# Kernel tuning notes

Measured on AMD Instinct MI355X. Metric: run time of the kernel, lower is better.

The kernel has to match this reference:

```python
import jax, jax.numpy as jnp
import numpy as np

N = 50000   # nodes
E = 600000  # edges / hyperedge incidences
D = 128     # node_in_dim
H = 128     # hidden_dim
TAU = 0.5
ALPHA = 0.5
LAM = 0.5

_PARAM_SHAPES = [('Wq0', (1, H)), ('bq0', (H,)), ('W0', (D, H)), ('b0', (H,)),
                 ('Whq0', (1, H)), ('bhq0', (H,)), ('Wh0', (D, H)), ('bh0', (H,)),
                 ('Wf0', (H, H)), ('bf0', (H,)), ('Wfh0', (H, H)), ('bfh0', (H,)),
                 ('aq0', (H,)), ('a0', (H,)), ('ahq0', (H,)), ('ah0', (H,)),
                 ('aq_', (H,)), ('a_', (H,)), ('ahq_', (H,)), ('ah_', (H,)),
                 ('Wlq', (1, H)), ('blq', (H,)), ('Wlf', (D, H)), ('blf', (H,)),
                 ('Wm1', (H, H)), ('bm1', (H,)), ('Wm2', (H, H)), ('bm2', (H,))]


def setup_inputs() -> dict:
    key = jax.random.key(0)
    ks = jax.random.split(key, 8 + len(_PARAM_SHAPES))
    inp = {}
    inp['feats'] = jax.random.normal(ks[0], (N, D), dtype=jnp.float32)
    inp['edge_index'] = jax.random.randint(ks[1], (2, E), 0, N).astype(jnp.int32)
    inp['edge_index_aug'] = jax.random.randint(ks[2], (2, E), 0, N).astype(jnp.int32)
    inp['pos'] = jax.random.randint(ks[3], (100,), 1, N).astype(jnp.int32)
    inp['q'] = 0
    for i, (nm, sh) in enumerate(_PARAM_SHAPES):
        inp[nm] = jax.random.normal(ks[4 + i], sh, dtype=jnp.float32) * 0.05
    return inp


def _forward(feats, Wq0, bq0, W0, b0, Whq0, bhq0, Wh0, bh0, Wf0, bf0, Wfh0, bfh0,
             aq0, a0, ahq0, ah0, aq_, a_, ahq_, ah_, Wlq, blq, Wlf, blf,
             Wm1, bm1, Wm2, bm2, edge_index, edge_index_aug, q, pos):
    # ---- GCNConv (PyG default: add self-loops + symmetric normalization) ----
    sl = jnp.arange(N, dtype=edge_index.dtype)
    src = jnp.concatenate([edge_index[0], sl])
    dst = jnp.concatenate([edge_index[1], sl])
    deg = jax.ops.segment_sum(jnp.ones(src.shape[0], jnp.float32), dst, num_segments=N)
    dinv = jax.lax.rsqrt(deg)  # deg >= 1 thanks to self-loops
    enorm = dinv[src] * dinv[dst]

    def gcn(x, W, b):
        xw = x @ W
        return jax.ops.segment_sum(xw[src] * enorm[:, None], dst, num_segments=N) + b

    # ---- HypergraphConv (PyG, no attention): X' = D^-1 H B^-1 H^T X W ----
    node = edge_index_aug[0]
    he = edge_index_aug[1]
    Be = jax.ops.segment_sum(jnp.ones((E,), jnp.float32), he, num_segments=N)
    Dn = jax.ops.segment_sum(jnp.ones((E,), jnp.float32), node, num_segments=N)
    Binv = jnp.where(Be > 0, 1.0 / Be, 0.0)
    Dninv = jnp.where(Dn > 0, 1.0 / Dn, 0.0)

    def hg(x, W, b):
        xw = x @ W
        me = jax.ops.segment_sum(xw[node], he, num_segments=N) * Binv[:, None]
        return jax.ops.segment_sum(me[he], node, num_segments=N) * Dninv[:, None] + b

    # ---- attention-weighted fusion of two views (softmax over 2 logits) ----
    def fuse(a, b, wa, wb):
        att = jax.nn.softmax(jnp.stack([a @ wa, b @ wb], axis=1), axis=1)  # [N,2]
        return att[:, 0:1] * a + att[:, 1:2] * b

    querys = jnp.zeros((N, 1), jnp.float32).at[q].set(1.0)
    hq = jax.nn.relu(gcn(querys, Wq0, bq0))
    h = jax.nn.relu(gcn(feats, W0, b0))
    hf = fuse(hq, h, aq0, a0)
    h_augq = jax.nn.relu(hg(querys, Whq0, bhq0))
    h_aug = jax.nn.relu(hg(feats, Wh0, bh0))
    h_augf = fuse(h_augq, h_aug, ahq0, ah0)
    querys2 = querys @ Wlq + blq
    feats2 = feats @ Wlf + blf
    hf_ = fuse(querys2, feats2, aq_, a_)
    hf = jax.nn.relu(hf + gcn(hf_, Wf0, bf0))
    hfh_ = fuse(querys2, feats2, ahq_, ah_)
    h_augf = jax.nn.relu(h_augf + hg(hfh_, Wfh0, bfh0))

    def mlp(x):
        return jax.nn.relu(x @ Wm1 + bm1) @ Wm2 + bm2

    z = mlp(hf)
    z_aug = mlp(h_augf)

    # ---- Contra loss ----
    def expcos(v, M):
        num = M @ v
        den = jnp.maximum(jnp.linalg.norm(M, axis=1) * jnp.linalg.norm(v), 1e-8)
        return jnp.exp(num / den / TAU)

    sim1 = expcos(z[q], z)
    sim_aug1 = expcos(z_aug[q], z_aug)
    sim2 = expcos(z[q], z_aug)
    sim_aug2 = expcos(z_aug[q], z)
    mask = jnp.zeros((N,), bool).at[pos].set(True).at[q].set(False)
    nmask = jnp.sum(mask).astype(jnp.float32)

    def nlm(s):  # mean over positives of -log(s_i / sum(s))
        r = jnp.log(jnp.sum(s)) - jnp.log(s)
        return jnp.sum(jnp.where(mask, r, 0.0)) / nmask

    loss_intra = 0.5 * (nlm(sim1) + nlm(sim_aug1))
    loss_inter = 0.5 * (nlm(sim2) + nlm(sim_aug2))
    z_unsup = jnp.log(jnp.sum(sim2)) - jnp.log(sim2[q])
    z_aug_unsup = jnp.log(jnp.sum(sim_aug2)) - jnp.log(sim_aug2[q])
    loss_unsup = 0.5 * z_unsup + 0.5 * z_aug_unsup
    return loss_intra + ALPHA * loss_inter + LAM * loss_unsup


def reference(feats, Wq0, bq0, W0, b0, Whq0, bhq0, Wh0, bh0, Wf0, bf0, Wfh0, bfh0,
              aq0, a0, ahq0, ah0, aq_, a_, ahq_, ah_, Wlq, blq, Wlf, blf,
              Wm1, bm1, Wm2, bm2, edge_index, edge_index_aug, q, pos):
    return _forward(feats, Wq0, bq0, W0, b0, Whq0, bhq0, Wh0, bh0, Wf0, bf0, Wfh0, bfh0,
                    aq0, a0, ahq0, ah0, aq_, a_, ahq_, ah_, Wlq, blq, Wlf, blf,
                    Wm1, bm1, Wm2, bm2, edge_index, edge_index_aug, q, pos)
```

## Files before the change

### kernel.cpp

```cpp
#include <hip/hip_runtime.h>

#define NN 50000
#define EE 600000
#define HH 128
#define TAU_INV 2.0f
#define PSZ 6250
#define CAP 48

typedef __attribute__((ext_vector_type(8))) short short8;
typedef __attribute__((ext_vector_type(4))) float f32x4;
typedef __attribute__((ext_vector_type(2))) float floatx2;

__device__ __forceinline__ float wsum64(float v) {
#pragma unroll
  for (int m = 32; m >= 1; m >>= 1) v += __shfl_xor(v, m, 64);
  return v;
}
__device__ __forceinline__ unsigned short f2bf(float f) {
  unsigned u = __builtin_bit_cast(unsigned, f);
  u = u + 0x7FFFu + ((u >> 16) & 1u);
  return (unsigned short)(u >> 16);
}
__device__ __forceinline__ float bf2f(unsigned short h) {
  unsigned u = ((unsigned)h) << 16;
  return __builtin_bit_cast(float, u);
}
__device__ __forceinline__ unsigned char fp8_enc1(float v) {
  int p = __builtin_amdgcn_cvt_pk_fp8_f32(v, v, 0, false);
  return (unsigned char)(p & 0xFF);
}
__device__ __forceinline__ void fp8x8_dec(uint2 v, float* f) {
  floatx2 a = __builtin_amdgcn_cvt_pk_f32_fp8(v.x, false);
  floatx2 b = __builtin_amdgcn_cvt_pk_f32_fp8(v.x, true);
  floatx2 c = __builtin_amdgcn_cvt_pk_f32_fp8(v.y, false);
  floatx2 d = __builtin_amdgcn_cvt_pk_f32_fp8(v.y, true);
  f[0] = a.x; f[1] = a.y; f[2] = b.x; f[3] = b.y;
  f[4] = c.x; f[5] = c.y; f[6] = d.x; f[7] = d.y;
}
__device__ __forceinline__ uint2 fp8x8_enc(const float* f) {
  int w0 = __builtin_amdgcn_cvt_pk_fp8_f32(f[0], f[1], 0, false);
  w0 = __builtin_amdgcn_cvt_pk_fp8_f32(f[2], f[3], w0, true);
  int w1 = __builtin_amdgcn_cvt_pk_fp8_f32(f[4], f[5], 0, false);
  w1 = __builtin_amdgcn_cvt_pk_fp8_f32(f[6], f[7], w1, true);
  return make_uint2((unsigned)w0, (unsigned)w1);
}

__global__ void fill_k(const int* __restrict__ ei, const int* __restrict__ ea,
                       const int* __restrict__ qp, int* __restrict__ cursor,
                       unsigned short* __restrict__ slotsA, unsigned short* __restrict__ slotsB,
                       unsigned short* __restrict__ slotsC, float* __restrict__ cntq) {
  const int p = blockIdx.x & 7;
  const int lo = p * PSZ, hi = lo + PSZ;
  const int q = *qp;
  const int stride = (gridDim.x >> 3) * 256;
  for (int e = (blockIdx.x >> 3) * 256 + threadIdx.x; e < EE; e += stride) {
    int src = ei[e], dst = ei[EE + e];
    if (dst >= lo && dst < hi) {
      int idx = atomicAdd(&cursor[dst], 1);
      if (idx < CAP) slotsA[dst * CAP + idx] = (unsigned short)src;
    }
    int node = ea[e], he = ea[EE + e];
    if (he >= lo && he < hi) {
      int idx = atomicAdd(&cursor[NN + he], 1);
      if (idx < CAP) slotsB[he * CAP + idx] = (unsigned short)node;
      if (node == q) atomicAdd(&cntq[he], 1.0f);
    }
    if (node >= lo && node < hi) {
      int idx = atomicAdd(&cursor[2 * NN + node], 1);
      if (idx < CAP) slotsC[node * CAP + idx] = (unsigned short)he;
    }
  }
}

__global__ void derive_k(const int* __restrict__ cursor, float* __restrict__ dinv,
                         float* __restrict__ Binv, float* __restrict__ Dninv,
                         const int* __restrict__ pos, const int* __restrict__ qp,
                         int* __restrict__ maskI) {
  int i = blockIdx.x * 256 + threadIdx.x;
  if (i < NN) {
    dinv[i] = rsqrtf((float)(cursor[i] + 1));
    int b = cursor[NN + i];
    Binv[i] = (b > 0) ? 1.0f / (float)b : 0.0f;
    int d = cursor[2 * NN + i];
    Dninv[i] = (d > 0) ? 1.0f / (float)d : 0.0f;
  }
  if (blockIdx.x == 0) {
    int t = threadIdx.x;
    if (t < 100) maskI[pos[t]] = 1;
    __syncthreads();
    if (t == 0) maskI[*qp] = 0;
  }
}

__global__ void shq_k(const int* __restrict__ ei, const int* __restrict__ ea,
                      const int* __restrict__ qp, const float* __restrict__ dinv,
                      const float* __restrict__ Binv, const float* __restrict__ cntq,
                      float* __restrict__ s_hq, float* __restrict__ s_hgq) {
  int e = blockIdx.x * 256 + threadIdx.x;
  if (e >= EE) return;
  int q = *qp;
  int src = ei[e];
  if (src == q) {
    int dst = ei[EE + e];
    atomicAdd(&s_hq[dst], dinv[q] * dinv[dst]);
  }
  int he = ea[EE + e];
  float cq = cntq[he];
  if (cq != 0.0f) {
    int node = ea[e];
    atomicAdd(&s_hgq[node], Binv[he] * cq);
  }
  if (e == 0) atomicAdd(&s_hq[q], dinv[q] * dinv[q]);
}

__global__ void pack_k(const float* __restrict__ W0, const float* __restrict__ Wh0,
                       const float* __restrict__ Wlf, const float* __restrict__ Wf0,
                       const float* __restrict__ Wfh0, const float* __restrict__ Wm1,
                       const float* __restrict__ Wm2, unsigned short* __restrict__ out) {
  int tid = blockIdx.x * 256 + threadIdx.x;
  if (tid >= 7 * 2048) return;
  int mat = tid >> 11, r = tid & 2047;
  int s = r >> 9, c = (r >> 6) & 7, lane = r & 63;
  const float* W = (mat == 0) ? W0 : (mat == 1) ? Wh0 : (mat == 2) ? Wlf
                 : (mat == 3) ? Wf0 : (mat == 4) ? Wfh0 : (mat == 5) ? Wm1 : Wm2;
  int k0 = 32 * s + (lane >> 4) * 8;
  int n = 16 * c + (lane & 15);
  unsigned short* o = out + (size_t)tid * 8;
#pragma unroll
  for (int j = 0; j < 8; ++j) o[j] = f2bf(W[(k0 + j) * 128 + n]);
}

#define LDSW 136

template <bool BIAS, bool RELU, int OM>
__device__ __forceinline__ void gemm_core(const unsigned short* As, const short8* Wp,
                                          const float* bias, void* outv, int r0, int nrows,
                                          int tid) {
  const int wave = tid >> 6, lane = tid & 63;
  const int quad = lane >> 4, l15 = lane & 15;
  const int rw = r0 + wave * 16;
  f32x4 acc[8];
#pragma unroll
  for (int c = 0; c < 8; ++c) acc[c] = (f32x4){0.f, 0.f, 0.f, 0.f};
#pragma unroll
  for (int s = 0; s < 4; ++s) {
    short8 a = *(const short8*)&As[(wave * 16 + l15) * LDSW + s * 32 + quad * 8];
#pragma unroll
    for (int c = 0; c < 8; ++c) {
      short8 b = Wp[(s * 8 + c) * 64 + lane];
      acc[c] = __builtin_amdgcn_mfma_f32_16x16x32_bf16(a, b, acc[c], 0, 0, 0);
    }
  }
#pragma unroll
  for (int c = 0; c < 8; ++c) {
    int col = c * 16 + l15;
    float bv = BIAS ? bias[col] : 0.f;
#pragma unroll
    for (int r = 0; r < 4; ++r) {
      int grow = rw + quad * 4 + r;
      if (grow < nrows) {
        float v = acc[c][r] + bv;
        if (RELU) v = fmaxf(v, 0.f);
        if (OM == 2)
          ((unsigned char*)outv)[(size_t)grow * 256 + col] = fp8_enc1(v);
        else if (OM == 1)
          ((unsigned short*)outv)[(size_t)grow * 128 + col] = f2bf(v);
        else
          ((float*)outv)[(size_t)grow * 128 + col] = v;
      }
    }
  }
}

__device__ __forceinline__ void stage_bf16(const unsigned short* A, unsigned short* As,
                                           int r0, int nrows, int tid) {
#pragma unroll
  for (int t = 0; t < 4; ++t) {
    int v = t * 256 + tid;
    int row = v >> 4, cc = v & 15;
    int gr = r0 + row;
    uint4 val = make_uint4(0, 0, 0, 0);
    if (gr < nrows) val = ((const uint4*)A)[(size_t)gr * 16 + cc];
    *(uint4*)&As[row * LDSW + cc * 8] = val;
  }
}

template <bool BIAS, bool RELU, int OM>
__global__ __launch_bounds__(256) void gemm2_mfma(const unsigned short* __restrict__ A0,
                                                  const unsigned short* __restrict__ A1,
                                                  const short8* __restrict__ Wp0,
                                                  const short8* __restrict__ Wp1,
                                                  const float* __restrict__ b0,
                                                  const float* __restrict__ b1,
                                                  void* __restrict__ o0, void* __restrict__ o1,
                                                  int nrows, int nblk) {
  __shared__ unsigned short As[64 * LDSW];
  int b = blockIdx.x;
  const unsigned short* A = A0;
  const short8* Wp = Wp0;
  const float* bias = b0;
  void* o = o0;
  if (b >= nblk) {
    b -= nblk; A = A1; Wp = Wp1; bias = b1; o = o1;
  }
  const int r0 = b * 64;
  stage_bf16(A, As, r0, nrows, threadIdx.x);
  __syncthreads();
  gemm_core<BIAS, RELU, OM>(As, Wp, bias, o, r0, nrows, threadIdx.x);
}

__global__ __launch_bounds__(256) void gemm3_mfma(const float* __restrict__ A,
                                                  const short8* __restrict__ Wp,
                                                  const float* __restrict__ bias2,
                                                  unsigned char* __restrict__ p1,
                                                  unsigned char* __restrict__ p2,
                                                  unsigned short* __restrict__ out2,
                                                  int nrows) {
  __shared__ unsigned short As[64 * LDSW];
  const int tid = threadIdx.x;
  const int r0 = blockIdx.x * 64;
#pragma unroll
  for (int t = 0; t < 8; ++t) {
    int v = t * 256 + tid;
    int row = v >> 5, c4 = v & 31;
    int gr = r0 + row;
    float4 val = make_float4(0.f, 0.f, 0.f, 0.f);
    if (gr < nrows) val = ((const float4*)A)[(size_t)gr * 32 + c4];
    ushort4 o;
    o.x = f2bf(val.x); o.y = f2bf(val.y); o.z = f2bf(val.z); o.w = f2bf(val.w);
    *(ushort4*)&As[row * LDSW + c4 * 4] = o;
  }
  __syncthreads();
  const int wave = tid >> 6, lane = tid & 63;
  const int quad = lane >> 4, l15 = lane & 15;
  const int rw = r0 + wave * 16;
  f32x4 acc[3][8];
#pragma unroll
  for (int m = 0; m < 3; ++m)
#pragma unroll
    for (int c = 0; c < 8; ++c) acc[m][c] = (f32x4){0.f, 0.f, 0.f, 0.f};
#pragma unroll
  for (int s = 0; s < 4; ++s) {
    short8 a = *(const short8*)&As[(wave * 16 + l15) * LDSW + s * 32 + quad * 8];
#pragma unroll
    for (int m = 0; m < 3; ++m)
#pragma unroll
      for (int c = 0; c < 8; ++c) {
        short8 b = Wp[(size_t)m * 2048 + (s * 8 + c) * 64 + lane];
        acc[m][c] = __builtin_amdgcn_mfma_f32_16x16x32_bf16(a, b, acc[m][c], 0, 0, 0);
      }
  }
#pragma unroll
  for (int c = 0; c < 8; ++c) {
    int col = c * 16 + l15;
    float bv = bias2[col];
#pragma unroll
    for (int r = 0; r < 4; ++r) {
      int grow = rw + quad * 4 + r;
      if (grow < nrows) {
        p1[(size_t)grow * 256 + col] = fp8_enc1(acc[0][c][r]);
        p2[(size_t)grow * 256 + col] = fp8_enc1(acc[1][c][r]);
        out2[(size_t)grow * 128 + col] = f2bf(acc[2][c][r] + bv);
      }
    }
  }
}

template <int MODE, bool OUTFP8>
__device__ __forceinline__ void gpair_body(const uint2* __restrict__ xp,
                                           unsigned short* __restrict__ y1,
                                           unsigned short* __restrict__ y2,
                                           uint2* __restrict__ yp,
                                           const int* __restrict__ cnt,
                                           const unsigned short* __restrict__ slots,
                                           const float* __restrict__ wv, int blk) {
  int node = blk * 8 + (threadIdx.x >> 5);
  if (node >= NN) return;
  int l = threadIdx.x & 31;
  int st = node * CAP;
  int n = min(cnt[node], CAP);
  float acc[8];
#pragma unroll
  for (int i = 0; i < 8; ++i) acc[i] = 0.f;
  int p = 0;
  for (; p + 4 <= n; p += 4) {
    ushort4 s4 = *(const ushort4*)&slots[st + p];
    uint2 v0 = xp[(size_t)s4.x * 32 + l];
    uint2 v1 = xp[(size_t)s4.y * 32 + l];
    uint2 v2 = xp[(size_t)s4.z * 32 + l];
    uint2 v3 = xp[(size_t)s4.w * 32 + l];
    float f[8];
    if (MODE == 0) {
      float w0 = wv[s4.x], w1 = wv[s4.y], w2 = wv[s4.z], w3 = wv[s4.w];
      fp8x8_dec(v0, f);
#pragma unroll
      for (int i = 0; i < 8; ++i) acc[i] = fmaf(w0, f[i], acc[i]);
      fp8x8_dec(v1, f);
#pragma unroll
      for (int i = 0; i < 8; ++i) acc[i] = fmaf(w1, f[i], acc[i]);
      fp8x8_dec(v2, f);
#pragma unroll
      for (int i = 0; i < 8; ++i) acc[i] = fmaf(w2, f[i], acc[i]);
      fp8x8_dec(v3, f);
#pragma unroll
      for (int i = 0; i < 8; ++i) acc[i] = fmaf(w3, f[i], acc[i]);
    } else {
      fp8x8_dec(v0, f);
#pragma unroll
      for (int i = 0; i < 8; ++i) acc[i] += f[i];
      fp8x8_dec(v1, f);
#pragma unroll
      for (int i = 0; i < 8; ++i) acc[i] += f[i];
      fp8x8_dec(v2, f);
#pragma unroll
      for (int i = 0; i < 8; ++i) acc[i] += f[i];
      fp8x8_dec(v3, f);
#pragma unroll
      for (int i = 0; i < 8; ++i) acc[i] += f[i];
    }
  }
  for (; p < n; ++p) {
    int s = slots[st + p];
    uint2 v = xp[(size_t)s * 32 + l];
    float f[8];
    fp8x8_dec(v, f);
    if (MODE == 0) {
      float w = wv[s];
#pragma unroll
      for (int i = 0; i < 8; ++i) acc[i] = fmaf(w, f[i], acc[i]);
    } else {
#pragma unroll
      for (int i = 0; i < 8; ++i) acc[i] += f[i];
    }
  }
  float sc = wv[node];
  if (MODE == 0) {
    uint2 v = xp[(size_t)node * 32 + l];
    float f[8];
    fp8x8_dec(v, f);
#pragma unroll
    for (int i = 0; i < 8; ++i) acc[i] = sc * fmaf(sc, f[i], acc[i]);
  } else {
#pragma unroll
    for (int i = 0; i < 8; ++i) acc[i] *= sc;
  }
  if (OUTFP8) {
    yp[(size_t)node * 32 + l] = fp8x8_enc(acc);
  } else {
    unsigned short* y = (l < 16) ? y1 : y2;
    int cg = l & 15;
    uint4 o;
    o.x = ((unsigned)f2bf(acc[1]) << 16) | f2bf(acc[0]);
    o.y = ((unsigned)f2bf(acc[3]) << 16) | f2bf(acc[2]);
    o.z = ((unsigned)f2bf(acc[5]) << 16) | f2bf(acc[4]);
    o.w = ((unsigned)f2bf(acc[7]) << 16) | f2bf(acc[6]);
    *(uint4*)&y[(size_t)node * 128 + cg * 8] = o;
  }
}

__global__ void dgather12_k(const uint2* __restrict__ xp1, unsigned short* __restrict__ y1a,
                            unsigned short* __restrict__ y1b, const uint2* __restrict__ xp2,
                            uint2* __restrict__ yp3, const int* __restrict__ cursor,
                            const unsigned short* __restrict__ slotsA,
                            const unsigned short* __restrict__ slotsB,
                            const float* __restrict__ dinv, const float* __restrict__ Binv,
                            int nblk) {
  int b = blockIdx.x;
  if (b < nblk)
    gpair_body<0, false>(xp1, y1a, y1b, nullptr, cursor, slotsA, dinv, b);
  else
    gpair_body<1, true>(xp2, nullptr, nullptr, yp3, cursor + NN, slotsB, Binv, b - nblk);
}

__global__ void dgather3_k(const uint2* __restrict__ xp, unsigned short* __restrict__ y1,
                           unsigned short* __restrict__ y2, const int* __restrict__ cursor,
                           const unsigned short* __restrict__ slotsC,
                           const float* __restrict__ wv) {
  gpair_body<1, false>(xp, y1, y2, nullptr, cursor + 2 * NN, slotsC, wv, blockIdx.x);
}

__device__ __forceinline__ void fuse_add_body(const unsigned short* __restrict__ g,
                                              const unsigned short* __restrict__ gr,
                                              const float* __restrict__ svec,
                                              const float* __restrict__ dscale,
                                              const float* __restrict__ Wq,
                                              const float* __restrict__ bq,
                                              const float* __restrict__ bm,
                                              const float* __restrict__ aq,
                                              const float* __restrict__ am,
                                              const float* __restrict__ bres,
                                              unsigned short* __restrict__ out, int blk) {
  int row = blk * 4 + (threadIdx.x >> 6);
  if (row >= NN) return;
  int lane = threadIdx.x & 63;
  int c0 = lane, c1 = lane + 64;
  float s = svec[row];
  if (dscale) s *= dscale[row];
  float hq0 = fmaxf(fmaf(s, Wq[c0], bq[c0]), 0.f);
  float hq1 = fmaxf(fmaf(s, Wq[c1], bq[c1]), 0.f);
  float h0 = fmaxf(bf2f(g[(size_t)row * 128 + c0]) + bm[c0], 0.f);
  float h1 = fmaxf(bf2f(g[(size_t)row * 128 + c1]) + bm[c1], 0.f);
  float dq = wsum64(hq0 * aq[c0] + hq1 * aq[c1]);
  float dm = wsum64(h0 * am[c0] + h1 * am[c1]);
  float mx = fmaxf(dq, dm);
  float e0 = expf(dq - mx), e1 = expf(dm - mx);
  float w0 = e0 / (e0 + e1), w1 = 1.f - w0;
  float r0 = fmaxf(w0 * hq0 + w1 * h0 + bf2f(gr[(size_t)row * 128 + c0]) + bres[c0], 0.f);
  float r1 = fmaxf(w0 * hq1 + w1 * h1 + bf2f(gr[(size_t)row * 128 + c1]) + bres[c1], 0.f);
  out[(size_t)row * 128 + c0] = f2bf(r0);
  out[(size_t)row * 128 + c1] = f2bf(r1);
}

__global__ void fuse_add2_k(const unsigned short* gA, const unsigned short* grA,
                            const float* svA, const float* dsA, const float* WqA,
                            const float* bqA, const float* bmA, const float* aqA,
                            const float* amA, const float* brA, unsigned short* outA,
                            const unsigned short* gB, const unsigned short* grB,
                            const float* svB, const float* dsB, const float* WqB,
                            const float* bqB, const float* bmB, const float* aqB,
                            const float* amB, const float* brB, unsigned short* outB,
                            int nblk) {
  int b = blockIdx.x;
  if (b < nblk)
    fuse_add_body(gA, grA, svA, dsA, WqA, bqA, bmA, aqA, amA, brA, outA, b);
  else
    fuse_add_body(gB, grB, svB, dsB, WqB, bqB, bmB, aqB, amB, brB, outB, b - nblk);
}

__global__ void fuse2_k(const unsigned short* __restrict__ f2, const int* __restrict__ qp,
                        const float* __restrict__ Wlq, const float* __restrict__ blq,
                        const float* __restrict__ aq1, const float* __restrict__ a1,
                        const float* __restrict__ aq2, const float* __restrict__ a2,
                        unsigned short* __restrict__ out1, unsigned short* __restrict__ out2) {
  int row = blockIdx.x * 4 + (threadIdx.x >> 6);
  if (row >= NN) return;
  int lane = threadIdx.x & 63;
  int c0 = lane, c1 = lane + 64;
  int q = *qp;
  float q20 = blq[c0] + ((row == q) ? Wlq[c0] : 0.f);
  float q21 = blq[c1] + ((row == q) ? Wlq[c1] : 0.f);
  float f0 = bf2f(f2[(size_t)row * 128 + c0]);
  float f1 = bf2f(f2[(size_t)row * 128 + c1]);
  float dq1 = wsum64(q20 * aq1[c0] + q21 * aq1[c1]);
  float df1 = wsum64(f0 * a1[c0] + f1 * a1[c1]);
  float dq2 = wsum64(q20 * aq2[c0] + q21 * aq2[c1]);
  float df2 = wsum64(f0 * a2[c0] + f1 * a2[c1]);
  {
    float mx = fmaxf(dq1, df1);
    float e0 = expf(dq1 - mx), e1 = expf(df1 - mx);
    float w0 = e0 / (e0 + e1), w1 = 1.f - w0;
    out1[(size_t)row * 128 + c0] = f2bf(w0 * q20 + w1 * f0);
    out1[(size_t)row * 128 + c1] = f2bf(w0 * q21 + w1 * f1);
  }
  {
    float mx = fmaxf(dq2, df2);
    float e0 = expf(dq2 - mx), e1 = expf(df2 - mx);
    float w0 = e0 / (e0 + e1), w1 = 1.f - w0;
    out2[(size_t)row * 128 + c0] = f2bf(w0 * q20 + w1 * f0);
    out2[(size_t)row * 128 + c1] = f2bf(w0 * q21 + w1 * f1);
  }
}

__global__ void sim_k(const unsigned short* __restrict__ z,
                      const unsigned short* __restrict__ za, const int* __restrict__ qp,
                      float4* __restrict__ simbuf, float* __restrict__ scal_out) {
  int row = blockIdx.x * 4 + (threadIdx.x >> 6);
  if (row >= NN) return;
  int lane = threadIdx.x & 63;
  int c0 = lane, c1 = lane + 64;
  int q = *qp;
  float zi0 = bf2f(z[(size_t)row * 128 + c0]), zi1 = bf2f(z[(size_t)row * 128 + c1]);
  float zai0 = bf2f(za[(size_t)row * 128 + c0]), zai1 = bf2f(za[(size_t)row * 128 + c1]);
  float zq0 = bf2f(z[(size_t)q * 128 + c0]), zq1 = bf2f(z[(size_t)q * 128 + c1]);
  float zaq0 = bf2f(za[(size_t)q * 128 + c0]), zaq1 = bf2f(za[(size_t)q * 128 + c1]);
  float nzi = wsum64(zi0 * zi0 + zi1 * zi1);
  float nzai = wsum64(zai0 * zai0 + zai1 * zai1);
  float nzq = wsum64(zq0 * zq0 + zq1 * zq1);
  float nzaq = wsum64(zaq0 * zaq0 + zaq1 * zaq1);
  float d1 = wsum64(zi0 * zq0 + zi1 * zq1);
  float d2 = wsum64(zai0 * zaq0 + zai1 * zaq1);
  float d3 = wsum64(zai0 * zq0 + zai1 * zq1);
  float d4 = wsum64(zi0 * zaq0 + zi1 * zaq1);
  if (lane == 0) {
    float ni = sqrtf(nzi), nai = sqrtf(nzai);
    float nq = sqrtf(nzq), naq = sqrtf(nzaq);
    float c1_ = d1 / fmaxf(ni * nq, 1e-8f) * TAU_INV;
    float ca1 = d2 / fmaxf(nai * naq, 1e-8f) * TAU_INV;
    float c2_ = d3 / fmaxf(nai * nq, 1e-8f) * TAU_INV;
    float ca2 = d4 / fmaxf(ni * naq, 1e-8f) * TAU_INV;
    simbuf[row] = make_float4(c1_, ca1, c2_, ca2);
    if (row == q) {
      scal_out[9] = c2_;
      scal_out[10] = ca2;
    }
  }
}

__global__ __launch_bounds__(256) void reduce_sim_k(const float4* __restrict__ simbuf,
                                                    const int* __restrict__ maskI,
                                                    float* __restrict__ scal) {
  float acc[9];
#pragma unroll
  for (int i = 0; i < 9; ++i) acc[i] = 0.f;
  for (int row = blockIdx.x * 256 + threadIdx.x; row < NN; row += gridDim.x * 256) {
    float4 v = simbuf[row];
    acc[0] += expf(v.x);
    acc[1] += expf(v.y);
    acc[2] += expf(v.z);
    acc[3] += expf(v.w);
    if (maskI[row]) {
      acc[4] += v.x; acc[5] += v.y; acc[6] += v.z; acc[7] += v.w;
      acc[8] += 1.0f;
    }
  }
  __shared__ float s[9][4];
  int lane = threadIdx.x & 63, wv = threadIdx.x >> 6;
#pragma unroll
  for (int i = 0; i < 9; ++i) {
    float r = wsum64(acc[i]);
    if (lane == 0) s[i][wv] = r;
  }
  __syncthreads();
  if (threadIdx.x < 9) {
    float r = s[threadIdx.x][0] + s[threadIdx.x][1] + s[threadIdx.x][2] + s[threadIdx.x][3];
    atomicAdd(&scal[threadIdx.x], r);
  }
}

__global__ void final_k(const float* __restrict__ scal, float* __restrict__ out) {
  if (threadIdx.x != 0 || blockIdx.x != 0) return;
  float S1 = scal[0], Sa1 = scal[1], S2 = scal[2], Sa2 = scal[3];
  float L1 = scal[4], La1 = scal[5], L2 = scal[6], La2 = scal[7];
  float NM = scal[8], Q2 = scal[9], Qa2 = scal[10];
  float intra = 0.5f * ((logf(S1) - L1 / NM) + (logf(Sa1) - La1 / NM));
  float inter = 0.5f * ((logf(S2) - L2 / NM) + (logf(Sa2) - La2 / NM));
  float unsup = 0.5f * (logf(S2) - Q2) + 0.5f * (logf(Sa2) - Qa2);
  out[0] = intra + 0.5f * inter + 0.5f * unsup;
}

extern "C" void kernel_launch(void* const* d_in, const int* in_sizes, int n_in,
                              void* d_out, int out_size, void* d_ws, size_t ws_size,
                              hipStream_t stream) {
  const float* feats = (const float*)d_in[0];
  const int* ei = (const int*)d_in[1];
  const int* ea = (const int*)d_in[2];
  const int* pos = (const int*)d_in[3];
  const int* qp = (const int*)d_in[4];
  const float* Wq0 = (const float*)d_in[5];
  const float* bq0 = (const float*)d_in[6];
  const float* W0 = (const float*)d_in[7];
  const float* b0 = (const float*)d_in[8];
  const float* Whq0 = (const float*)d_in[9];
  const float* bhq0 = (const float*)d_in[10];
  const float* Wh0 = (const float*)d_in[11];
  const float* bh0 = (const float*)d_in[12];
  const float* Wf0 = (const float*)d_in[13];
  const float* bf0 = (const float*)d_in[14];
  const float* Wfh0 = (const float*)d_in[15];
  const float* bfh0 = (const float*)d_in[16];
  const float* aq0 = (const float*)d_in[17];
  const float* a0 = (const float*)d_in[18];
  const float* ahq0 = (const float*)d_in[19];
  const float* ah0 = (const float*)d_in[20];
  const float* aq_ = (const float*)d_in[21];
  const float* a_ = (const float*)d_in[22];
  const float* ahq_ = (const float*)d_in[23];
  const float* ah_ = (const float*)d_in[24];
  const float* Wlq = (const float*)d_in[25];
  const float* blq = (const float*)d_in[26];
  const float* Wlf = (const float*)d_in[27];
  const float* blf = (const float*)d_in[28];
  const float* Wm1 = (const float*)d_in[29];
  const float* bm1 = (const float*)d_in[30];
  const float* Wm2 = (const float*)d_in[31];
  const float* bm2 = (const float*)d_in[32];

  char* ws = (char*)d_ws;
  size_t off = 0;
  auto take = [&](size_t bytes) -> void* {
    void* p = ws + off;
    off = (off + bytes + 255) & ~(size_t)255;
    return p;
  };
  int* cursor3 = (int*)take(3 * NN * 4);
  int* maskI = (int*)take(NN * 4);
  float* s_hq = (float*)take(NN * 4);
  float* cntq = (float*)take(NN * 4);
  float* s_hgq = (float*)take(NN * 4);
  float* scal = (float*)take(64 * 4);
  size_t zero_end = off;
  unsigned short* slotsA = (unsigned short*)take((size_t)NN * CAP * 2);
  unsigned short* slotsB = (unsigned short*)take((size_t)NN * CAP * 2);
  unsigned short* slotsC = (unsigned short*)take((size_t)NN * CAP * 2);
  float* dinv = (float*)take(NN * 4);
  float* Binv = (float*)take(NN * 4);
  float* Dninv = (float*)take(NN * 4);
  float4* simbuf = (float4*)take((size_t)NN * 16);
  unsigned short* Wpack = (unsigned short*)take((size_t)7 * 16384 * 2);
  const size_t BFSZ = (size_t)NN * HH * 2;
  unsigned short* B0 = (unsigned short*)take(BFSZ);
  unsigned short* B1 = (unsigned short*)take(BFSZ);
  unsigned short* B2 = (unsigned short*)take(BFSZ);
  unsigned short* B3 = (unsigned short*)take(BFSZ);
  unsigned short* B4 = (unsigned short*)take(BFSZ);
  unsigned short* B5 = (unsigned short*)take(BFSZ);
  unsigned short* B6 = (unsigned short*)take(BFSZ);
  unsigned char* P1 = (unsigned char*)take((size_t)NN * 256);
  unsigned char* P2 = (unsigned char*)take((size_t)NN * 256);
  unsigned char* P3 = (unsigned char*)take((size_t)NN * 256);

  const int NB = (NN + 255) / 256;
  const int EB = (EE + 255) / 256;
  const int GMB = (NN + 63) / 64;
  const int GTB = (NN + 7) / 8;
  const int RB = (NN + 3) / 4;
  const short8* Wp = (const short8*)Wpack;

  hipMemsetAsync(d_ws, 0, zero_end, stream);
  fill_k<<<4096, 256, 0, stream>>>(ei, ea, qp, cursor3, slotsA, slotsB, slotsC, cntq);
  derive_k<<<NB, 256, 0, stream>>>(cursor3, dinv, Binv, Dninv, pos, qp, maskI);
  shq_k<<<EB, 256, 0, stream>>>(ei, ea, qp, dinv, Binv, cntq, s_hq, s_hgq);

  pack_k<<<(7 * 2048 + 255) / 256, 256, 0, stream>>>(W0, Wh0, Wlf, Wf0, Wfh0, Wm1, Wm2,
                                                     Wpack);
  gemm3_mfma<<<GMB, 256, 0, stream>>>(feats, Wp, blf, P1, P2, B6, NN);
  fuse2_k<<<RB, 256, 0, stream>>>(B6, qp, Wlq, blq, aq_, a_, ahq_, ah_, B3, B4);
  gemm2_mfma<false, false, 2><<<2 * GMB, 256, 0, stream>>>(
      B3, B4, Wp + (size_t)3 * 2048, Wp + (size_t)4 * 2048, nullptr, nullptr, P1 + 128,
      P2 + 128, NN, GMB);
  dgather12_k<<<2 * GTB, 256, 0, stream>>>((const uint2*)P1, B0, B1, (const uint2*)P2,
                                           (uint2*)P3, cursor3, slotsA, slotsB, dinv, Binv,
                                           GTB);
  dgather3_k<<<GTB, 256, 0, stream>>>((const uint2*)P3, B2, B5, cursor3, slotsC, Dninv);
  fuse_add2_k<<<2 * RB, 256, 0, stream>>>(
      B0, B1, s_hq, nullptr, Wq0, bq0, b0, aq0, a0, bf0, B3,
      B2, B5, s_hgq, Dninv, Whq0, bhq0, bh0, ahq0, ah0, bfh0, B4, RB);
  gemm2_mfma<true, true, 1><<<2 * GMB, 256, 0, stream>>>(
      B3, B4, Wp + (size_t)5 * 2048, Wp + (size_t)5 * 2048, bm1, bm1, B0, B1, NN, GMB);
  gemm2_mfma<true, false, 1><<<2 * GMB, 256, 0, stream>>>(
      B0, B1, Wp + (size_t)6 * 2048, Wp + (size_t)6 * 2048, bm2, bm2, B2, B5, NN, GMB);
  sim_k<<<RB, 256, 0, stream>>>(B2, B5, qp, simbuf, scal);
  reduce_sim_k<<<64, 256, 0, stream>>>(simbuf, maskI, scal);
  final_k<<<1, 64, 0, stream>>>(scal, (float*)d_out);
}
```

Baseline: 477.1 us.

## Merge independent stages into shared launches and pad slot stride to 64

Independent stages now share launches so they overlap on the device: weight packing with edge-slot filling, the feature GEMM with degree derivation and the query-score pass, the third gather with the first fuse-add, and the second fuse-add with the first MLP GEMM. The query-score pass now derives its normalization from the cursor counts directly, so it no longer has to wait for a separate derive kernel. The MLP GEMMs are rescheduled into a staggered pipeline, and the RELU flag becomes a runtime argument. The per-node slot stride is padded from 48 to 64 entries for aligned gather rows. The aim is to cut launch count and idle tails; the cost is more branching inside kernels, heterogeneous blocks sharing a grid, and a larger slot buffer.

Result: no change. 477.2 us (+0.0%).

```diff
diff --git a/kernel.cpp b/kernel.cpp
--- a/kernel.cpp
+++ b/kernel.cpp
@@ -6,6 +6,7 @@
 #define TAU_INV 2.0f
 #define PSZ 6250
 #define CAP 48
+#define SSTR 64
 
 typedef __attribute__((ext_vector_type(8))) short short8;
 typedef __attribute__((ext_vector_type(4))) float f32x4;
@@ -45,79 +46,48 @@
   return make_uint2((unsigned)w0, (unsigned)w1);
 }
 
-__global__ void fill_k(const int* __restrict__ ei, const int* __restrict__ ea,
-                       const int* __restrict__ qp, int* __restrict__ cursor,
-                       unsigned short* __restrict__ slotsA, unsigned short* __restrict__ slotsB,
-                       unsigned short* __restrict__ slotsC, float* __restrict__ cntq) {
-  const int p = blockIdx.x & 7;
+#define LDSW 136
+
+
+__device__ __forceinline__ void fill_body(const int* __restrict__ ei,
+                                          const int* __restrict__ ea,
+                                          const int* __restrict__ qp, int* __restrict__ cursor,
+                                          unsigned short* __restrict__ slotsA,
+                                          unsigned short* __restrict__ slotsB,
+                                          unsigned short* __restrict__ slotsC,
+                                          float* __restrict__ cntq, int blk, int nblk) {
+  const int p = blk & 7;
   const int lo = p * PSZ, hi = lo + PSZ;
   const int q = *qp;
-  const int stride = (gridDim.x >> 3) * 256;
-  for (int e = (blockIdx.x >> 3) * 256 + threadIdx.x; e < EE; e += stride) {
+  const int stride = (nblk >> 3) * 256;
+  for (int e = (blk >> 3) * 256 + threadIdx.x; e < EE; e += stride) {
     int src = ei[e], dst = ei[EE + e];
     if (dst >= lo && dst < hi) {
       int idx = atomicAdd(&cursor[dst], 1);
-      if (idx < CAP) slotsA[dst * CAP + idx] = (unsigned short)src;
+      if (idx < CAP) slotsA[dst * SSTR + idx] = (unsigned short)src;
     }
     int node = ea[e], he = ea[EE + e];
     if (he >= lo && he < hi) {
       int idx = atomicAdd(&cursor[NN + he], 1);
-      if (idx < CAP) slotsB[he * CAP + idx] = (unsigned short)node;
+      if (idx < CAP) slotsB[he * SSTR + idx] = (unsigned short)node;
       if (node == q) atomicAdd(&cntq[he], 1.0f);
     }
     if (node >= lo && node < hi) {
       int idx = atomicAdd(&cursor[2 * NN + node], 1);
-      if (idx < CAP) slotsC[node * CAP + idx] = (unsigned short)he;
-    }
-  }
-}
-
-__global__ void derive_k(const int* __restrict__ cursor, float* __restrict__ dinv,
-                         float* __restrict__ Binv, float* __restrict__ Dninv,
-                         const int* __restrict__ pos, const int* __restrict__ qp,
-                         int* __restrict__ maskI) {
-  int i = blockIdx.x * 256 + threadIdx.x;
-  if (i < NN) {
-    dinv[i] = rsqrtf((float)(cursor[i] + 1));
-    int b = cursor[NN + i];
-    Binv[i] = (b > 0) ? 1.0f / (float)b : 0.0f;
-    int d = cursor[2 * NN + i];
-    Dninv[i] = (d > 0) ? 1.0f / (float)d : 0.0f;
-  }
-  if (blockIdx.x == 0) {
-    int t = threadIdx.x;
-    if (t < 100) maskI[pos[t]] = 1;
-    __syncthreads();
-    if (t == 0) maskI[*qp] = 0;
-  }
-}
-
-__global__ void shq_k(const int* __restrict__ ei, const int* __restrict__ ea,
-                      const int* __restrict__ qp, const float* __restrict__ dinv,
-                      const float* __restrict__ Binv, const float* __restrict__ cntq,
-                      float* __restrict__ s_hq, float* __restrict__ s_hgq) {
-  int e = blockIdx.x * 256 + threadIdx.x;
-  if (e >= EE) return;
-  int q = *qp;
-  int src = ei[e];
-  if (src == q) {
-    int dst = ei[EE + e];
-    atomicAdd(&s_hq[dst], dinv[q] * dinv[dst]);
-  }
-  int he = ea[EE + e];
-  float cq = cntq[he];
-  if (cq != 0.0f) {
-    int node = ea[e];
-    atomicAdd(&s_hgq[node], Binv[he] * cq);
-  }
-  if (e == 0) atomicAdd(&s_hq[q], dinv[q] * dinv[q]);
-}
-
-__global__ void pack_k(const float* __restrict__ W0, const float* __restrict__ Wh0,
-                       const float* __restrict__ Wlf, const float* __restrict__ Wf0,
-                       const float* __restrict__ Wfh0, const float* __restrict__ Wm1,
-                       const float* __restrict__ Wm2, unsigned short* __restrict__ out) {
-  int tid = blockIdx.x * 256 + threadIdx.x;
+      if (idx < CAP) slotsC[node * SSTR + idx] = (unsigned short)he;
+    }
+  }
+}
+
+__device__ __forceinline__ void pack_body(const float* __restrict__ W0,
+                                          const float* __restrict__ Wh0,
+                                          const float* __restrict__ Wlf,
+                                          const float* __restrict__ Wf0,
+                                          const float* __restrict__ Wfh0,
+                                          const float* __restrict__ Wm1,
+                                          const float* __restrict__ Wm2,
+                                          unsigned short* __restrict__ out, int blk) {
+  int tid = blk * 256 + threadIdx.x;
   if (tid >= 7 * 2048) return;
   int mat = tid >> 11, r = tid & 2047;
   int s = r >> 9, c = (r >> 6) & 7, lane = r & 63;
@@ -130,12 +100,56 @@
   for (int j = 0; j < 8; ++j) o[j] = f2bf(W[(k0 + j) * 128 + n]);
 }
 
-#define LDSW 136
-
-template <bool BIAS, bool RELU, int OM>
-__device__ __forceinline__ void gemm_core(const unsigned short* As, const short8* Wp,
-                                          const float* bias, void* outv, int r0, int nrows,
-                                          int tid) {
+__device__ __forceinline__ void derive_body(const int* __restrict__ cursor,
+                                            float* __restrict__ dinv, float* __restrict__ Binv,
+                                            float* __restrict__ Dninv,
+                                            const int* __restrict__ pos,
+                                            const int* __restrict__ qp,
+                                            int* __restrict__ maskI, int blk) {
+  int i = blk * 256 + threadIdx.x;
+  if (i < NN) {
+    dinv[i] = rsqrtf((float)(cursor[i] + 1));
+    int b = cursor[NN + i];
+    Binv[i] = (b > 0) ? 1.0f / (float)b : 0.0f;
+    int d = cursor[2 * NN + i];
+    Dninv[i] = (d > 0) ? 1.0f / (float)d : 0.0f;
+  }
+  if (blk == 0) {
+    int t = threadIdx.x;
+    if (t < 100) maskI[pos[t]] = 1;
+    __syncthreads();
+    if (t == 0) maskI[*qp] = 0;
+  }
+}
+
+__device__ __forceinline__ void shq_body(const int* __restrict__ ei, const int* __restrict__ ea,
+                                         const int* __restrict__ qp,
+                                         const int* __restrict__ cursor,
+                                         const float* __restrict__ cntq,
+                                         float* __restrict__ s_hq, float* __restrict__ s_hgq,
+                                         int blk) {
+  int e = blk * 256 + threadIdx.x;
+  if (e >= EE) return;
+  int q = *qp;
+  int src = ei[e];
+  if (src == q) {
+    int dst = ei[EE + e];
+    float dq = rsqrtf((float)(cursor[q] + 1));
+    atomicAdd(&s_hq[dst], dq * rsqrtf((float)(cursor[dst] + 1)));
+  }
+  int he = ea[EE + e];
+  float cq = cntq[he];
+  if (cq != 0.0f) {
+    int node = ea[e];
+    atomicAdd(&s_hgq[node], cq / (float)cursor[NN + he]);
+  }
+  if (e == 0) atomicAdd(&s_hq[q], 1.0f / (float)(cursor[q] + 1));
+}
+
+template <bool BIAS, int OM>
+__device__ __forceinline__ void gemm_core_rt(const unsigned short* As, const short8* Wp,
+                                             const float* bias, void* outv, int r0, int nrows,
+                                             int tid, int relu) {
   const int wave = tid >> 6, lane = tid & 63;
   const int quad = lane >> 4, l15 = lane & 15;
   const int rw = r0 + wave * 16;
@@ -160,13 +174,11 @@
       int grow = rw + quad * 4 + r;
       if (grow < nrows) {
         float v = acc[c][r] + bv;
-        if (RELU) v = fmaxf(v, 0.f);
+        if (relu) v = fmaxf(v, 0.f);
         if (OM == 2)
           ((unsigned char*)outv)[(size_t)grow * 256 + col] = fp8_enc1(v);
-        else if (OM == 1)
+        else
           ((unsigned short*)outv)[(size_t)grow * 128 + col] = f2bf(v);
-        else
-          ((float*)outv)[(size_t)grow * 128 + col] = v;
       }
     }
   }
@@ -185,40 +197,15 @@
   }
 }
 
-template <bool BIAS, bool RELU, int OM>
-__global__ __launch_bounds__(256) void gemm2_mfma(const unsigned short* __restrict__ A0,
-                                                  const unsigned short* __restrict__ A1,
-                                                  const short8* __restrict__ Wp0,
-                                                  const short8* __restrict__ Wp1,
-                                                  const float* __restrict__ b0,
-                                                  const float* __restrict__ b1,
-                                                  void* __restrict__ o0, void* __restrict__ o1,
-                                                  int nrows, int nblk) {
-  __shared__ unsigned short As[64 * LDSW];
-  int b = blockIdx.x;
-  const unsigned short* A = A0;
-  const short8* Wp = Wp0;
-  const float* bias = b0;
-  void* o = o0;
-  if (b >= nblk) {
-    b -= nblk; A = A1; Wp = Wp1; bias = b1; o = o1;
-  }
-  const int r0 = b * 64;
-  stage_bf16(A, As, r0, nrows, threadIdx.x);
-  __syncthreads();
-  gemm_core<BIAS, RELU, OM>(As, Wp, bias, o, r0, nrows, threadIdx.x);
-}
-
-__global__ __launch_bounds__(256) void gemm3_mfma(const float* __restrict__ A,
-                                                  const short8* __restrict__ Wp,
-                                                  const float* __restrict__ bias2,
-                                                  unsigned char* __restrict__ p1,
-                                                  unsigned char* __restrict__ p2,
-                                                  unsigned short* __restrict__ out2,
-                                                  int nrows) {
-  __shared__ unsigned short As[64 * LDSW];
+__device__ __forceinline__ void gemm3_body(unsigned short* As, const float* __restrict__ A,
+                                           const short8* __restrict__ Wp,
+                                           const float* __restrict__ bias2,
+                                           unsigned char* __restrict__ p1,
+                                           unsigned char* __restrict__ p2,
+                                           unsigned short* __restrict__ out2, int nrows,
+                                           int blk) {
   const int tid = threadIdx.x;
-  const int r0 = blockIdx.x * 64;
+  const int r0 = blk * 64;
 #pragma unroll
   for (int t = 0; t < 8; ++t) {
     int v = t * 256 + tid;
@@ -277,7 +264,7 @@
   int node = blk * 8 + (threadIdx.x >> 5);
   if (node >= NN) return;
   int l = threadIdx.x & 31;
-  int st = node * CAP;
+  int st = node * SSTR;
   int n = min(cnt[node], CAP);
   float acc[8];
 #pragma unroll
@@ -356,27 +343,6 @@
     o.w = ((unsigned)f2bf(acc[7]) << 16) | f2bf(acc[6]);
     *(uint4*)&y[(size_t)node * 128 + cg * 8] = o;
   }
-}
-
-__global__ void dgather12_k(const uint2* __restrict__ xp1, unsigned short* __restrict__ y1a,
-                            unsigned short* __restrict__ y1b, const uint2* __restrict__ xp2,
-                            uint2* __restrict__ yp3, const int* __restrict__ cursor,
-                            const unsigned short* __restrict__ slotsA,
-                            const unsigned short* __restrict__ slotsB,
-                            const float* __restrict__ dinv, const float* __restrict__ Binv,
-                            int nblk) {
-  int b = blockIdx.x;
-  if (b < nblk)
-    gpair_body<0, false>(xp1, y1a, y1b, nullptr, cursor, slotsA, dinv, b);
-  else
-    gpair_body<1, true>(xp2, nullptr, nullptr, yp3, cursor + NN, slotsB, Binv, b - nblk);
-}
-
-__global__ void dgather3_k(const uint2* __restrict__ xp, unsigned short* __restrict__ y1,
-                           unsigned short* __restrict__ y2, const int* __restrict__ cursor,
-                           const unsigned short* __restrict__ slotsC,
-                           const float* __restrict__ wv) {
-  gpair_body<1, false>(xp, y1, y2, nullptr, cursor + 2 * NN, slotsC, wv, blockIdx.x);
 }
 
 __device__ __forceinline__ void fuse_add_body(const unsigned short* __restrict__ g,
@@ -411,20 +377,36 @@
   out[(size_t)row * 128 + c1] = f2bf(r1);
 }
 
-__global__ void fuse_add2_k(const unsigned short* gA, const unsigned short* grA,
-                            const float* svA, const float* dsA, const float* WqA,
-                            const float* bqA, const float* bmA, const float* aqA,
-                            const float* amA, const float* brA, unsigned short* outA,
-                            const unsigned short* gB, const unsigned short* grB,
-                            const float* svB, const float* dsB, const float* WqB,
-                            const float* bqB, const float* bmB, const float* aqB,
-                            const float* amB, const float* brB, unsigned short* outB,
-                            int nblk) {
+
+__global__ __launch_bounds__(256) void fill_pack_k(
+    const int* ei, const int* ea, const int* qp, int* cursor, unsigned short* slotsA,
+    unsigned short* slotsB, unsigned short* slotsC, float* cntq, int fb, const float* W0,
+    const float* Wh0, const float* Wlf, const float* Wf0, const float* Wfh0, const float* Wm1,
+    const float* Wm2, unsigned short* Wpack) {
   int b = blockIdx.x;
-  if (b < nblk)
-    fuse_add_body(gA, grA, svA, dsA, WqA, bqA, bmA, aqA, amA, brA, outA, b);
+  if (b < fb)
+    fill_body(ei, ea, qp, cursor, slotsA, slotsB, slotsC, cntq, b, fb);
   else
-    fuse_add_body(gB, grB, svB, dsB, WqB, bqB, bmB, aqB, amB, brB, outB, b - nblk);
+    pack_body(W0, Wh0, Wlf, Wf0, Wfh0, Wm1, Wm2, Wpack, b - fb);
+}
+
+__global__ __launch_bounds__(256) void g3ds_k(
+    const float* A, const short8* Wp, const float* bias2, unsigned char* p1, unsigned char* p2,
+    unsigned short* out2, int gmb, const int* cursor, float* dinv, float* Binv, float* Dninv,
+    const int* pos, const int* qp, int* maskI, const int* ei, const int* ea, const float* cntq,
+    float* s_hq, float* s_hgq, int nb) {
+  __shared__ unsigned short As[64 * LDSW];
+  int b = blockIdx.x;
+  if (b < gmb) {
+    gemm3_body(As, A, Wp, bias2, p1, p2, out2, NN, b);
+    return;
+  }
+  b -= gmb;
+  if (b < nb) {
+    derive_body(cursor, dinv, Binv, Dninv, pos, qp, maskI, b);
+    return;
+  }
+  shq_body(ei, ea, qp, cursor, cntq, s_hq, s_hgq, b - nb);
 }
 
 __global__ void fuse2_k(const unsigned short* __restrict__ f2, const int* __restrict__ qp,
@@ -459,6 +441,88 @@
     out2[(size_t)row * 128 + c0] = f2bf(w0 * q20 + w1 * f0);
     out2[(size_t)row * 128 + c1] = f2bf(w0 * q21 + w1 * f1);
   }
+}
+
+__global__ __launch_bounds__(256) void gemm2f8_k(const unsigned short* A0,
+                                                 const unsigned short* A1, const short8* Wp0,
+                                                 const short8* Wp1, unsigned char* o0,
+                                                 unsigned char* o1, int nblk) {
+  __shared__ unsigned short As[64 * LDSW];
+  int b = blockIdx.x;
+  const unsigned short* A = A0;
+  const short8* Wp = Wp0;
+  unsigned char* o = o0;
+  if (b >= nblk) {
+    b -= nblk; A = A1; Wp = Wp1; o = o1;
+  }
+  stage_bf16(A, As, b * 64, NN, threadIdx.x);
+  __syncthreads();
+  gemm_core_rt<false, 2>(As, Wp, nullptr, o, b * 64, NN, threadIdx.x, 0);
+}
+
+__global__ void dgather12_k(const uint2* __restrict__ xp1, unsigned short* __restrict__ y1a,
+                            unsigned short* __restrict__ y1b, const uint2* __restrict__ xp2,
+                            uint2* __restrict__ yp3, const int* __restrict__ cursor,
+                            const unsigned short* __restrict__ slotsA,
+                            const unsigned short* __restrict__ slotsB,
+                            const float* __restrict__ dinv, const float* __restrict__ Binv,
+                            int nblk) {
+  int b = blockIdx.x;
+  if (b < nblk)
+    gpair_body<0, false>(xp1, y1a, y1b, nullptr, cursor, slotsA, dinv, b);
+  else
+    gpair_body<1, true>(xp2, nullptr, nullptr, yp3, cursor + NN, slotsB, Binv, b - nblk);
+}
+
+__global__ void g3fa_k(const uint2* xp, unsigned short* y1, unsigned short* y2,
+                       const int* cursor, const unsigned short* slotsC, const float* Dninv,
+                       int gtb, const unsigned short* g, const unsigned short* gr,
+                       const float* svec, const float* Wq, const float* bq, const float* bm,
+                       const float* aq, const float* am, const float* bres,
+                       unsigned short* out) {
+  int b = blockIdx.x;
+  if (b < gtb)
+    gpair_body<1, false>(xp, y1, y2, nullptr, cursor + 2 * NN, slotsC, Dninv, b);
+  else
+    fuse_add_body(g, gr, svec, nullptr, Wq, bq, bm, aq, am, bres, out, b - gtb);
+}
+
+__global__ __launch_bounds__(256) void fagemm_k(
+    const unsigned short* g, const unsigned short* gr, const float* svec, const float* dscale,
+    const float* Wq, const float* bq, const float* bm, const float* aq, const float* am,
+    const float* bres, unsigned short* out, int rb, const unsigned short* A, const short8* Wp,
+    const float* bias, unsigned short* o, int relu) {
+  __shared__ unsigned short As[64 * LDSW];
+  int b = blockIdx.x;
+  if (b < rb) {
+    fuse_add_body(g, gr, svec, dscale, Wq, bq, bm, aq, am, bres, out, b);
+    return;
+  }
+  b -= rb;
+  stage_bf16(A, As, b * 64, NN, threadIdx.x);
+  __syncthreads();
+  gemm_core_rt<true, 1>(As, Wp, bias, o, b * 64, NN, threadIdx.x, relu);
+}
+
+__global__ __launch_bounds__(256) void gemm2x_k(const unsigned short* A0,
+                                                const unsigned short* A1, const short8* Wp0,
+                                                const short8* Wp1, const float* b0,
+                                                const float* b1, unsigned short* o0,
+                                                unsigned short* o1, int nblk, int relu0,
+                                                int relu1) {
+  __shared__ unsigned short As[64 * LDSW];
+  int b = blockIdx.x;
+  const unsigned short* A = A0;
+  const short8* Wp = Wp0;
+  const float* bias = b0;
+  unsigned short* o = o0;
+  int relu = relu0;
+  if (b >= nblk) {
+    b -= nblk; A = A1; Wp = Wp1; bias = b1; o = o1; relu = relu1;
+  }
+  stage_bf16(A, As, b * 64, NN, threadIdx.x);
+  __syncthreads();
+  gemm_core_rt<true, 1>(As, Wp, bias, o, b * 64, NN, threadIdx.x, relu);
 }
 
 __global__ void sim_k(const unsigned short* __restrict__ z,
@@ -589,9 +653,9 @@
   float* s_hgq = (float*)take(NN * 4);
   float* scal = (float*)take(64 * 4);
   size_t zero_end = off;
-  unsigned short* slotsA = (unsigned short*)take((size_t)NN * CAP * 2);
-  unsigned short* slotsB = (unsigned short*)take((size_t)NN * CAP * 2);
-  unsigned short* slotsC = (unsigned short*)take((size_t)NN * CAP * 2);
+  unsigned short* slotsA = (unsigned short*)take((size_t)NN * SSTR * 2);
+  unsigned short* slotsB = (unsigned short*)take((size_t)NN * SSTR * 2);
+  unsigned short* slotsC = (unsigned short*)take((size_t)NN * SSTR * 2);
   float* dinv = (float*)take(NN * 4);
   float* Binv = (float*)take(NN * 4);
   float* Dninv = (float*)take(NN * 4);
@@ -614,31 +678,30 @@
   const int GMB = (NN + 63) / 64;
   const int GTB = (NN + 7) / 8;
   const int RB = (NN + 3) / 4;
+  const int FB = 4096;
+  const int PB = 56;
   const short8* Wp = (const short8*)Wpack;
 
   hipMemsetAsync(d_ws, 0, zero_end, stream);
-  fill_k<<<4096, 256, 0, stream>>>(ei, ea, qp, cursor3, slotsA, slotsB, slotsC, cntq);
-  derive_k<<<NB, 256, 0, stream>>>(cursor3, dinv, Binv, Dninv, pos, qp, maskI);
-  shq_k<<<EB, 256, 0, stream>>>(ei, ea, qp, dinv, Binv, cntq, s_hq, s_hgq);
-
-  pack_k<<<(7 * 2048 + 255) / 256, 256, 0, stream>>>(W0, Wh0, Wlf, Wf0, Wfh0, Wm1, Wm2,
-                                                     Wpack);
-  gemm3_mfma<<<GMB, 256, 0, stream>>>(feats, Wp, blf, P1, P2, B6, NN);
+  fill_pack_k<<<FB + PB, 256, 0, stream>>>(ei, ea, qp, cursor3, slotsA, slotsB, slotsC, cntq,
+                                           FB, W0, Wh0, Wlf, Wf0, Wfh0, Wm1, Wm2, Wpack);
+  g3ds_k<<<GMB + NB + EB, 256, 0, stream>>>(feats, Wp, blf, P1, P2, B6, GMB, cursor3, dinv,
+                                            Binv, Dninv, pos, qp, maskI, ei, ea, cntq, s_hq,
+                                            s_hgq, NB);
   fuse2_k<<<RB, 256, 0, stream>>>(B6, qp, Wlq, blq, aq_, a_, ahq_, ah_, B3, B4);
-  gemm2_mfma<false, false, 2><<<2 * GMB, 256, 0, stream>>>(
-      B3, B4, Wp + (size_t)3 * 2048, Wp + (size_t)4 * 2048, nullptr, nullptr, P1 + 128,
-      P2 + 128, NN, GMB);
+  gemm2f8_k<<<2 * GMB, 256, 0, stream>>>(B3, B4, Wp + (size_t)3 * 2048, Wp + (size_t)4 * 2048,
+                                         P1 + 128, P2 + 128, GMB);
   dgather12_k<<<2 * GTB, 256, 0, stream>>>((const uint2*)P1, B0, B1, (const uint2*)P2,
                                            (uint2*)P3, cursor3, slotsA, slotsB, dinv, Binv,
                                            GTB);
-  dgather3_k<<<GTB, 256, 0, stream>>>((const uint2*)P3, B2, B5, cursor3, slotsC, Dninv);
-  fuse_add2_k<<<2 * RB, 256, 0, stream>>>(
-      B0, B1, s_hq, nullptr, Wq0, bq0, b0, aq0, a0, bf0, B3,
-      B2, B5, s_hgq, Dninv, Whq0, bhq0, bh0, ahq0, ah0, bfh0, B4, RB);
-  gemm2_mfma<true, true, 1><<<2 * GMB, 256, 0, stream>>>(
-      B3, B4, Wp + (size_t)5 * 2048, Wp + (size_t)5 * 2048, bm1, bm1, B0, B1, NN, GMB);
-  gemm2_mfma<true, false, 1><<<2 * GMB, 256, 0, stream>>>(
-      B0, B1, Wp + (size_t)6 * 2048, Wp + (size_t)6 * 2048, bm2, bm2, B2, B5, NN, GMB);
+  g3fa_k<<<GTB + RB, 256, 0, stream>>>((const uint2*)P3, B2, B5, cursor3, slotsC, Dninv, GTB,
+                                       B0, B1, s_hq, Wq0, bq0, b0, aq0, a0, bf0, B3);
+  fagemm_k<<<RB + GMB, 256, 0, stream>>>(B2, B5, s_hgq, Dninv, Whq0, bhq0, bh0, ahq0, ah0,
+                                         bfh0, B4, RB, B3, Wp + (size_t)5 * 2048, bm1, B0, 1);
+  gemm2x_k<<<2 * GMB, 256, 0, stream>>>(B4, B0, Wp + (size_t)5 * 2048, Wp + (size_t)6 * 2048,
+                                        bm1, bm2, B1, B2, GMB, 1, 0);
+  gemm2x_k<<<GMB, 256, 0, stream>>>(B1, B1, Wp + (size_t)6 * 2048, Wp + (size_t)6 * 2048, bm2,
+                                    bm2, B5, B5, GMB, 0, 0);
   sim_k<<<RB, 256, 0, stream>>>(B2, B5, qp, simbuf, scal);
   reduce_sim_k<<<64, 256, 0, stream>>>(simbuf, maskI, scal);
   final_k<<<1, 64, 0, stream>>>(scal, (float*)d_out);
```
